# Performance work log

Hardware: AMD Instinct MI355X
Metric: run time of the kernel (lower is better)

## Reference

```python
import jax, jax.numpy as jnp
import numpy as np

SIZE = 768
SMALL = SIZE // 4 + 1  # 193
N_ROWS = 16 * 512      # 8192 flattened timesteps
N_CODES = 30000
N_PAIRS = 300000


def setup_inputs() -> dict:
    key = jax.random.key(0)
    ks = jax.random.split(key, 10)
    rnn_output = jax.random.normal(ks[0], (16, 512, SIZE), dtype=jnp.float32)
    weight = jax.random.normal(ks[1], (N_CODES, SIZE + 1), dtype=jnp.float32) * 0.02
    weight1 = jax.random.normal(ks[2], (N_CODES, SMALL), dtype=jnp.float32) * 0.02
    idx0 = jnp.stack([
        jax.random.randint(ks[3], (N_PAIRS,), 0, N_ROWS),
        jax.random.randint(ks[4], (N_PAIRS,), 0, N_CODES),
    ], axis=1).astype(jnp.int64)
    y0 = (jax.random.uniform(ks[5], (N_PAIRS,)) < 0.5).astype(jnp.float32)
    idx1 = jnp.stack([
        jax.random.randint(ks[6], (N_PAIRS,), 0, N_ROWS),
        jax.random.randint(ks[7], (N_PAIRS,), 0, N_CODES),
    ], axis=1).astype(jnp.int64)
    y1 = (jax.random.uniform(ks[8], (N_PAIRS,)) < 0.5).astype(jnp.float32)
    seen0 = jnp.zeros((N_PAIRS,), dtype=jnp.float32)
    seen1 = jnp.zeros((N_PAIRS,), dtype=jnp.float32)
    return {"rnn_output": rnn_output, "weight": weight, "weight1": weight1,
            "idx0": idx0, "y0": y0, "seen0": seen0,
            "idx1": idx1, "y1": y1, "seen1": seen1}


def _embedding_dot(features, table, idx):
    # gather feature rows and code-embedding rows, then row-wise dot -> [N]
    f = features[idx[:, 0]]   # [N, D]
    w = table[idx[:, 1]]      # [N, D]
    return jnp.sum(f * w, axis=-1)


def _bce_logits_sum(logits, targets):
    # stable: log(1 + exp(x)) - x*y, summed
    return jnp.sum(jnp.logaddexp(jnp.float32(0.0), logits) - logits * targets)


def reference(rnn_output, weight, weight1, idx0, y0, seen0, idx1, y1, seen1):
    flat = rnn_output.reshape(-1, SIZE)                     # [B*T, size]
    bias = jnp.ones((flat.shape[0], 1), dtype=flat.dtype)
    rnn_with_bias = jnp.concatenate([flat, bias], axis=1)   # [B*T, size+1]

    final = _embedding_dot(rnn_with_bias, weight, idx0)     # [N]
    loss = _bce_logits_sum(final, y0)

    smaller = rnn_with_bias[:, -SMALL:]                     # [B*T, small]
    final1 = _embedding_dot(smaller, weight1, idx1)         # [N]
    loss1 = _bce_logits_sum(final1, y1)

    return final, loss + loss1
```

## Files before the change

### kernel.cpp

```cpp
#include <hip/hip_runtime.h>
#include <hip/hip_fp16.h>

#define FSIZE   768
#define TW0     769
#define TW1     193
#define COL1    576
#define NPAIRS  300000
#define NCODES  30000
#define NROWS   8192
#define NCB     32768

#define NB0     1176
#define NB1     1176
#define NGRID   (NB0 + NB1)
#define NPART   NGRID

#define PB_H    512
#define PB_F    512
#define PB_W0   1024
#define PB_W1   256
#define NPRE    (PB_H + PB_F + PB_W0 + PB_W1)
#define S_H     (PB_H)
#define S_F     (PB_H + PB_F)
#define S_W0    (PB_H + PB_F + PB_W0)
#define FEAT_U4 393216
#define W0_U4   1440000
#define W1_U4   360000

#define O_FEAT8  ((size_t)0)
#define O_W08    (O_FEAT8 + 1572864)
#define O_W18    (O_W08 + 5760000)
#define O_B0F    (O_W18 + 1440000)
#define O_B1F    (O_B0F + 30000)
#define O_CNT    (O_B1F + 30000)
#define O_CUR    (O_CNT + 65536)
#define O_SREC   (O_CUR + 65536)
#define O_PART   (O_SREC + 2400000)
#define WS_U32   (O_PART + NPART + 64)

#define FSCALE   16.0f
#define WSCALE   64.0f
#define DESCALE  (1.0f / 1024.0f)

typedef float f32x2_t __attribute__((ext_vector_type(2)));

__device__ __forceinline__ float loss_term(float x, float y) {
    float ax = fabsf(x);
    return fmaxf(x, 0.0f) + log1pf(__expf(-ax)) - x * y;
}

__device__ __forceinline__ float4 ld4u(const float* p) {
    float4 v; __builtin_memcpy(&v, p, 16); return v;
}

#if defined(__has_builtin)
# if __has_builtin(__builtin_amdgcn_cvt_pk_f32_fp8)
#  define HW_FP8_DEC 1
# endif
# if __has_builtin(__builtin_amdgcn_cvt_pk_fp8_f32)
#  define HW_FP8_ENC 1
# endif
#endif

__device__ __forceinline__ float sw_fp8_to_f32(unsigned b) {
    unsigned mag = b & 0x7fu;
    unsigned r = ((b & 0x80u) << 24) | ((mag << 20) + 0x3C000000u);
    float f = __uint_as_float(r);
    return mag ? f : 0.0f;
}

template <bool HI>
__device__ __forceinline__ f32x2_t fp8x2_to_f32(unsigned u) {
#ifdef HW_FP8_DEC
    return __builtin_amdgcn_cvt_pk_f32_fp8(u, HI);
#else
    f32x2_t o;
    unsigned lo8 = HI ? ((u >> 16) & 0xffu) : (u & 0xffu);
    unsigned hi8 = HI ? ((u >> 24) & 0xffu) : ((u >> 8) & 0xffu);
    o[0] = sw_fp8_to_f32(lo8);
    o[1] = sw_fp8_to_f32(hi8);
    return o;
#endif
}

__device__ __forceinline__ unsigned sw_f32_to_fp8(float x) {
    unsigned short h = __half_as_ushort(__float2half(x));
    unsigned s = ((unsigned)h >> 8) & 0x80u;
    int e = (h >> 10) & 31;
    unsigned m = h & 1023u;
    if (e >= 23) return s | 0x7eu;
    if (e < 9)  return s;
    unsigned t = ((unsigned)(e - 8) << 3) | (m >> 7);
    unsigned rnd = (m >> 6) & 1u, sticky = (m & 63u) ? 1u : 0u;
    t += (rnd & (sticky | (t & 1u)));
    if (t > 0x7eu) t = 0x7eu;
    return s | t;
}

__device__ __forceinline__ unsigned f32x4_to_fp8(float a, float b, float c, float d) {
#ifdef HW_FP8_ENC
    int u = __builtin_amdgcn_cvt_pk_fp8_f32(a, b, 0, false);
    u = __builtin_amdgcn_cvt_pk_fp8_f32(c, d, u, true);
    return (unsigned)u;
#else
    return sw_f32_to_fp8(a) | (sw_f32_to_fp8(b) << 8)
         | (sw_f32_to_fp8(c) << 16) | (sw_f32_to_fp8(d) << 24);
#endif
}

__device__ __forceinline__ uint4 enc16(const float* s, float sc) {
    float4 a = ld4u(s), b = ld4u(s + 4), c = ld4u(s + 8), d = ld4u(s + 12);
    uint4 o;
    o.x = f32x4_to_fp8(a.x * sc, a.y * sc, a.z * sc, a.w * sc);
    o.y = f32x4_to_fp8(b.x * sc, b.y * sc, b.z * sc, b.w * sc);
    o.z = f32x4_to_fp8(c.x * sc, c.y * sc, c.z * sc, c.w * sc);
    o.w = f32x4_to_fp8(d.x * sc, d.y * sc, d.z * sc, d.w * sc);
    return o;
}

__device__ __forceinline__ float dot16(uint4 u, const float* w, float s) {
    f32x2_t p;
    p = fp8x2_to_f32<false>(u.x); s += p[0] * w[0]  + p[1] * w[1];
    p = fp8x2_to_f32<true >(u.x); s += p[0] * w[2]  + p[1] * w[3];
    p = fp8x2_to_f32<false>(u.y); s += p[0] * w[4]  + p[1] * w[5];
    p = fp8x2_to_f32<true >(u.y); s += p[0] * w[6]  + p[1] * w[7];
    p = fp8x2_to_f32<false>(u.z); s += p[0] * w[8]  + p[1] * w[9];
    p = fp8x2_to_f32<true >(u.z); s += p[0] * w[10] + p[1] * w[11];
    p = fp8x2_to_f32<false>(u.w); s += p[0] * w[12] + p[1] * w[13];
    p = fp8x2_to_f32<true >(u.w); s += p[0] * w[14] + p[1] * w[15];
    return s;
}

__device__ __forceinline__ float dot8(uint2 u, const float* w, float s) {
    f32x2_t p;
    p = fp8x2_to_f32<false>(u.x); s += p[0] * w[0] + p[1] * w[1];
    p = fp8x2_to_f32<true >(u.x); s += p[0] * w[2] + p[1] * w[3];
    p = fp8x2_to_f32<false>(u.y); s += p[0] * w[4] + p[1] * w[5];
    p = fp8x2_to_f32<true >(u.y); s += p[0] * w[6] + p[1] * w[7];
    return s;
}

__device__ __forceinline__ void unpack16(uint4 u, float* w) {
    f32x2_t p;
    p = fp8x2_to_f32<false>(u.x); w[0]  = p[0]; w[1]  = p[1];
    p = fp8x2_to_f32<true >(u.x); w[2]  = p[0]; w[3]  = p[1];
    p = fp8x2_to_f32<false>(u.y); w[4]  = p[0]; w[5]  = p[1];
    p = fp8x2_to_f32<true >(u.y); w[6]  = p[0]; w[7]  = p[1];
    p = fp8x2_to_f32<false>(u.z); w[8]  = p[0]; w[9]  = p[1];
    p = fp8x2_to_f32<true >(u.z); w[10] = p[0]; w[11] = p[1];
    p = fp8x2_to_f32<false>(u.w); w[12] = p[0]; w[13] = p[1];
    p = fp8x2_to_f32<true >(u.w); w[14] = p[0]; w[15] = p[1];
}

__device__ __forceinline__ void unpack8(uint2 u, float* w) {
    f32x2_t p;
    p = fp8x2_to_f32<false>(u.x); w[0] = p[0]; w[1] = p[1];
    p = fp8x2_to_f32<true >(u.x); w[2] = p[0]; w[3] = p[1];
    p = fp8x2_to_f32<false>(u.y); w[4] = p[0]; w[5] = p[1];
    p = fp8x2_to_f32<true >(u.y); w[6] = p[0]; w[7] = p[1];
}

__global__ __launch_bounds__(256) void zero_cnt_kernel(int* __restrict__ cnt) {
    cnt[blockIdx.x * 256 + threadIdx.x] = 0;
}

__global__ __launch_bounds__(256) void fused_pre_kernel(
    const float* __restrict__ feat, const float* __restrict__ w0,
    const float* __restrict__ w1,
    const int* __restrict__ idx0, const int* __restrict__ idx1,
    uint4* __restrict__ feat8, uint4* __restrict__ w08, uint4* __restrict__ w18,
    float* __restrict__ b0f, float* __restrict__ b1f, int* __restrict__ cnt)
{
    const int bid = blockIdx.x;
    if (bid < S_H) {
        const int tid = bid * 256 + threadIdx.x;
#pragma unroll
        for (int k = 0; k < 5; ++k) {
            const int i = tid + k * (PB_H * 256);
            if (i < 2 * NPAIRS) {
                if (i < NPAIRS) atomicAdd(&cnt[idx0[2 * i + 1]], 1);
                else            atomicAdd(&cnt[NCB + idx1[2 * (i - NPAIRS) + 1]], 1);
            }
        }
    } else if (bid < S_F) {
        const int tid = (bid - S_H) * 256 + threadIdx.x;
#pragma unroll
        for (int k = 0; k < 3; ++k) {
            const int i = tid + k * (PB_F * 256);
            feat8[i] = enc16(feat + (size_t)i * 16, FSCALE);
        }
    } else if (bid < S_W0) {
        const int tid = (bid - S_F) * 256 + threadIdx.x;
#pragma unroll
        for (int k = 0; k < 6; ++k) {
            const int i = tid + k * (PB_W0 * 256);
            if (i < W0_U4) {
                const int c = i / 48;
                const int e = (i - c * 48) * 16;
                const float* src = w0 + (size_t)c * TW0 + e;
                w08[i] = enc16(src, WSCALE);
                if (e == 0) b0f[c] = src[FSIZE];
            }
        }
    } else {
        const int tid = (bid - S_W0) * 256 + threadIdx.x;
#pragma unroll
        for (int k = 0; k < 6; ++k) {
            const int i = tid + k * (PB_W1 * 256);
            if (i < W1_U4) {
                const int c = i / 12;
                const int e = (i - c * 12) * 16;
                const float* src = w1 + (size_t)c * TW1 + e;
                w18[i] = enc16(src, WSCALE);
                if (e == 0) b1f[c] = src[TW1 - 1];
            }
        }
    }
}

__global__ __launch_bounds__(1024) void scan2_kernel(const int* __restrict__ cnt,
                                                     int* __restrict__ cursor) {
    __shared__ int wsum[16];
    __shared__ int wbase[16];
    const int t = threadIdx.x;
    const int lane = t & 63, wv = t >> 6;
    const int4* c4 = (const int4*)cnt + (size_t)t * 16;
    int4 v[16];
#pragma unroll
    for (int j = 0; j < 16; ++j) v[j] = c4[j];
    int s = 0;
#pragma unroll
    for (int j = 0; j < 16; ++j) {
        int a;
        a = v[j].x; v[j].x = s; s += a;
        a = v[j].y; v[j].y = s; s += a;
        a = v[j].z; v[j].z = s; s += a;
        a = v[j].w; v[j].w = s; s += a;
    }
    int incl = s;
#pragma unroll
    for (int off = 1; off < 64; off <<= 1) {
        int u = __shfl_up(incl, off, 64);
        if (lane >= off) incl += u;
    }
    if (lane == 63) wsum[wv] = incl;
    __syncthreads();
    if (wv == 0 && lane < 16) {
        int mysum = wsum[lane];
        int winc = mysum;
#pragma unroll
        for (int off = 1; off < 16; off <<= 1) {
            int u = __shfl_up(winc, off, 64);
            if (lane >= off) winc += u;
        }
        wbase[lane] = winc - mysum;
    }
    __syncthreads();
    const int base = wbase[wv] + incl - s;
    int4* cu = (int4*)cursor + (size_t)t * 16;
#pragma unroll
    for (int j = 0; j < 16; ++j)
        cu[j] = make_int4(base + v[j].x, base + v[j].y, base + v[j].z, base + v[j].w);
}

__global__ __launch_bounds__(256) void scatter2_kernel(
    const int* __restrict__ idx0, const float* __restrict__ y0,
    const int* __restrict__ idx1, const float* __restrict__ y1,
    int* __restrict__ cursor, uint4* __restrict__ srec, float* __restrict__ loss_out)
{
    const int tid = blockIdx.x * 256 + threadIdx.x;
    if (tid == 0) loss_out[0] = 0.0f;
#pragma unroll
    for (int k = 0; k < 2; ++k) {
        const int t = tid + k * 300032;
        if (t < NPAIRS) {
            int r = idx0[2 * t], c = idx0[2 * t + 1];
            int pos = atomicAdd(&cursor[c], 1);
            srec[pos] = make_uint4((unsigned)r, (unsigned)c, __float_as_uint(y0[t]), (unsigned)t);
        } else if (t < 2 * NPAIRS) {
            int p = t - NPAIRS;
            int r = idx1[2 * p], c = idx1[2 * p + 1];
            int pos = atomicAdd(&cursor[NCB + c], 1);
            srec[pos] = make_uint4((unsigned)r, (unsigned)c, __float_as_uint(y1[p]), (unsigned)p);
        }
    }
}

__global__ __launch_bounds__(256) void main3_kernel(
    const unsigned char* __restrict__ feat8, const unsigned char* __restrict__ w08,
    const unsigned char* __restrict__ w18,
    const float* __restrict__ b0f, const float* __restrict__ b1f,
    const uint4* __restrict__ srec,
    float* __restrict__ out_final, float* __restrict__ loss_out)
{
    __shared__ float bsum[4];
    const int lane = threadIdx.x & 63;
    const int wv   = threadIdx.x >> 6;
    float wavesum = 0.f;

    if (blockIdx.x < NB0) {
        const int work = (blockIdx.x & 7) * (NB0 / 8) + (blockIdx.x >> 3);
        const int wid = work * 4 + wv;
        const int g = lane >> 4, sub = lane & 15;
        const int mypair = wid * 64 + 16 * g + sub;
        int rdidx = mypair < NPAIRS ? mypair : NPAIRS - 1;
        const uint4 rec = srec[rdidx];
        int prev_c = -1;
        float wc[48];
        float wb = 0.f, lg = 0.f;
#pragma unroll
        for (int j = 0; j < 16; ++j) {
            const bool valid = (wid * 64 + 16 * g + j) < NPAIRS;
            if (valid) {
                const int src = (lane & 48) | j;
                const int r = __shfl((int)rec.x, src, 64);
                const int c = __shfl((int)rec.y, src, 64);
                if (c != prev_c) {
                    prev_c = c;
                    const unsigned char* wr = w08 + (size_t)c * FSIZE + 48 * sub;
                    uint4 wu0 = *(const uint4*)wr;
                    uint4 wu1 = *(const uint4*)(wr + 16);
                    uint4 wu2 = *(const uint4*)(wr + 32);
                    unpack16(wu0, &wc[0]);
                    unpack16(wu1, &wc[16]);
                    unpack16(wu2, &wc[32]);
                    wb = b0f[c];
                }
                const unsigned char* fr = feat8 + (size_t)r * FSIZE + 48 * sub;
                uint4 f0 = *(const uint4*)fr;
                uint4 f1 = *(const uint4*)(fr + 16);
                uint4 f2 = *(const uint4*)(fr + 32);
                float s = dot16(f0, &wc[0], 0.f);
                s = dot16(f1, &wc[16], s);
                s = dot16(f2, &wc[32], s);
                s += __shfl_xor(s, 8, 64);
                s += __shfl_xor(s, 4, 64);
                s += __shfl_xor(s, 2, 64);
                s += __shfl_xor(s, 1, 64);
                lg = (sub == j) ? s * DESCALE + wb : lg;
            }
        }
        float ll = 0.f;
        if (mypair < NPAIRS) {
            out_final[rec.w] = lg;
            ll = loss_term(lg, __uint_as_float(rec.z));
        }
#pragma unroll
        for (int m = 32; m; m >>= 1) ll += __shfl_xor(ll, m, 64);
        wavesum = ll;
    } else {
        const int tb = blockIdx.x - NB0;
        const int work1 = (tb & 7) * (NB1 / 8) + (tb >> 3);
        const long base = (long)(work1 * 4 + wv) * 64;
        if (base < NPAIRS) {
            const int g = lane >> 3, sub = lane & 7;
            long lpos = base + 8 * g + sub;
            if (lpos > NPAIRS - 1) lpos = NPAIRS - 1;
            const uint4 rec = srec[(size_t)NPAIRS + lpos];
            int prev_c = -1;
            float wc[24];
            float wb = 0.f, lg = 0.f;
#pragma unroll
            for (int j = 0; j < 8; ++j) {
                const bool valid = (base + 8 * g + j) < NPAIRS;
                const int src = (lane & 56) | j;
                const int r = __shfl((int)rec.x, src, 64);
                const int c = __shfl((int)rec.y, src, 64);
                if (valid) {
                    if (c != prev_c) {
                        prev_c = c;
                        const unsigned char* wr = w18 + (size_t)c * 192 + 24 * sub;
                        uint2 wu0 = *(const uint2*)wr;
                        uint2 wu1 = *(const uint2*)(wr + 8);
                        uint2 wu2 = *(const uint2*)(wr + 16);
                        unpack8(wu0, &wc[0]);
                        unpack8(wu1, &wc[8]);
                        unpack8(wu2, &wc[16]);
                        wb = b1f[c];
                    }
                    const unsigned char* fr = feat8 + (size_t)r * FSIZE + COL1 + 24 * sub;
                    uint2 f0 = *(const uint2*)fr;
                    uint2 f1 = *(const uint2*)(fr + 8);
                    uint2 f2 = *(const uint2*)(fr + 16);
                    float s = dot8(f0, &wc[0], 0.f);
                    s = dot8(f1, &wc[8], s);
                    s = dot8(f2, &wc[16], s);
                    s += __shfl_xor(s, 4, 64);
                    s += __shfl_xor(s, 2, 64);
                    s += __shfl_xor(s, 1, 64);
                    lg = (sub == j) ? s * DESCALE + wb : lg;
                }
            }
            float ll = 0.f;
            if ((base + 8 * g + sub) < NPAIRS)
                ll = loss_term(lg, __uint_as_float(rec.z));
#pragma unroll
            for (int m = 32; m; m >>= 1) ll += __shfl_xor(ll, m, 64);
            wavesum = ll;
        }
    }

    if (lane == 0) bsum[wv] = wavesum;
    __syncthreads();
    if (threadIdx.x == 0) {
        float t = bsum[0] + bsum[1] + bsum[2] + bsum[3];
        atomicAdd(loss_out, t);
    }
}

__global__ __launch_bounds__(1024) void reduce_kernel(
    const float* __restrict__ partial, int n, float* __restrict__ out)
{
    __shared__ float sh[1024];
    float s = 0.0f;
    for (int i = threadIdx.x; i < n; i += 1024) s += partial[i];
    sh[threadIdx.x] = s;
    __syncthreads();
    for (int off = 512; off; off >>= 1) {
        if ((int)threadIdx.x < off) sh[threadIdx.x] += sh[threadIdx.x + off];
        __syncthreads();
    }
    if (threadIdx.x == 0) out[0] = sh[0];
}

__global__ __launch_bounds__(256) void task0_kernel(
    const float* __restrict__ feat, const float* __restrict__ wt,
    const int* __restrict__ idx, const float* __restrict__ y,
    float* __restrict__ out_final, float* __restrict__ partial)
{
    __shared__ float lsum[4];
    const int lane = threadIdx.x & 63;
    const int wv = threadIdx.x >> 6;
    const int pair = blockIdx.x * 4 + wv;
    const int r = idx[2 * pair];
    const int c = idx[2 * pair + 1];
    const float4* f4 = (const float4*)(feat + (size_t)r * FSIZE);
    const float* wrow = wt + (size_t)c * TW0;
    float s = 0.0f;
#pragma unroll
    for (int k = 0; k < 3; ++k) {
        const int j = lane + (k << 6);
        float4 f = f4[j];
        float4 w = ld4u(wrow + 4 * j);
        s += f.x * w.x + f.y * w.y + f.z * w.z + f.w * w.w;
    }
#pragma unroll
    for (int m = 32; m; m >>= 1) s += __shfl_xor(s, m, 64);
    if (lane == 0) {
        const float logit = s + wrow[FSIZE];
        out_final[pair] = logit;
        lsum[wv] = loss_term(logit, y[pair]);
    }
    __syncthreads();
    if (threadIdx.x == 0)
        partial[blockIdx.x] = lsum[0] + lsum[1] + lsum[2] + lsum[3];
}

__global__ __launch_bounds__(256) void task1_kernel(
    const float* __restrict__ feat, const float* __restrict__ wt,
    const int* __restrict__ idx, const float* __restrict__ y,
    float* __restrict__ partial)
{
    __shared__ float lsum[16];
    const int lane = threadIdx.x & 63;
    const int wv = threadIdx.x >> 6;
    const int sub = lane & 15;
    const int pg = lane >> 4;
    const int pair = (blockIdx.x * 4 + wv) * 4 + pg;
    const int r = idx[2 * pair];
    const int c = idx[2 * pair + 1];
    const float4* f4 = (const float4*)(feat + (size_t)r * FSIZE + COL1);
    const float* wrow = wt + (size_t)c * TW1;
    float s = 0.0f;
#pragma unroll
    for (int k = 0; k < 3; ++k) {
        const int j = sub + (k << 4);
        float4 f = f4[j];
        float4 w = ld4u(wrow + 4 * j);
        s += f.x * w.x + f.y * w.y + f.z * w.z + f.w * w.w;
    }
#pragma unroll
    for (int m = 8; m; m >>= 1) s += __shfl_xor(s, m, 64);
    if (sub == 0) {
        const float logit = s + wrow[TW1 - 1];
        lsum[wv * 4 + pg] = loss_term(logit, y[pair]);
    }
    __syncthreads();
    if (threadIdx.x == 0) {
        float t = 0.0f;
#pragma unroll
        for (int i = 0; i < 16; ++i) t += lsum[i];
        partial[blockIdx.x] = t;
    }
}

extern "C" void kernel_launch(void* const* d_in, const int* in_sizes, int n_in,
                              void* d_out, int out_size, void* d_ws, size_t ws_size,
                              hipStream_t stream) {
    const float* feat = (const float*)d_in[0];
    const float* w0   = (const float*)d_in[1];
    const float* w1   = (const float*)d_in[2];
    const int*   idx0 = (const int*)d_in[3];
    const float* y0   = (const float*)d_in[4];
    const int*   idx1 = (const int*)d_in[6];
    const float* y1   = (const float*)d_in[7];

    float* out = (float*)d_out;
    unsigned* ws = (unsigned*)d_ws;

    if (ws_size >= WS_U32 * 4) {
        unsigned char* feat8 = (unsigned char*)(ws + O_FEAT8);
        unsigned char* w08   = (unsigned char*)(ws + O_W08);
        unsigned char* w18   = (unsigned char*)(ws + O_W18);
        float* b0f   = (float*)(ws + O_B0F);
        float* b1f   = (float*)(ws + O_B1F);
        int*   cnt   = (int*)(ws + O_CNT);
        int*   cursor= (int*)(ws + O_CUR);
        uint4* srec  = (uint4*)(ws + O_SREC);

        zero_cnt_kernel<<<256, 256, 0, stream>>>(cnt);
        fused_pre_kernel<<<NPRE, 256, 0, stream>>>(
            feat, w0, w1, idx0, idx1,
            (uint4*)feat8, (uint4*)w08, (uint4*)w18, b0f, b1f, cnt);
        scan2_kernel<<<1, 1024, 0, stream>>>(cnt, cursor);
        scatter2_kernel<<<1172, 256, 0, stream>>>(
            idx0, y0, idx1, y1, cursor, srec, out + NPAIRS);
        main3_kernel<<<NGRID, 256, 0, stream>>>(
            feat8, w08, w18, b0f, b1f, srec, out, out + NPAIRS);
    } else {
        float* part = (float*)ws;
        const int nb0 = NPAIRS / 4;
        const int nb1 = NPAIRS / 16;
        task0_kernel<<<nb0, 256, 0, stream>>>(feat, w0, idx0, y0, out, part);
        task1_kernel<<<nb1, 256, 0, stream>>>(feat, w1, idx1, y1, part + nb0);
        reduce_kernel<<<1, 1024, 0, stream>>>(part, nb0 + nb1, out + NPAIRS);
    }
}
```

Measured before the change: 167.5 us.

## Split preprocessing into two kernels and halve pairs per wave in task0

The fused preprocessing kernel is split in two. The histogram and feature encoding run before the scan, and weight encoding is moved after the scatter. Each thread now handles one element instead of looping, so the grids are larger. In the main kernel, task0 waves now process 32 pairs with 8 per 16-lane group instead of 64, and the block count doubles. This trades more weight-row reloads and less in-wave reuse for more parallelism and shorter serial loops, and adds one kernel launch.

```diff
diff --git a/kernel.cpp b/kernel.cpp
--- a/kernel.cpp
+++ b/kernel.cpp
@@ -10,21 +10,18 @@
 #define NROWS   8192
 #define NCB     32768
 
-#define NB0     1176
+#define NWAVES0 (NPAIRS / 32)
+#define NB0     2344
 #define NB1     1176
 #define NGRID   (NB0 + NB1)
 #define NPART   NGRID
 
-#define PB_H    512
-#define PB_F    512
-#define PB_W0   1024
-#define PB_W1   256
-#define NPRE    (PB_H + PB_F + PB_W0 + PB_W1)
-#define S_H     (PB_H)
-#define S_F     (PB_H + PB_F)
-#define S_W0    (PB_H + PB_F + PB_W0)
-#define FEAT_U4 393216
-#define W0_U4   1440000
+#define PA_H    1172
+#define PA_F    1536
+#define NPREA   (PA_H + PA_F)
+#define PB_W0   5625
+#define PB_W1   1407
+#define NPREB   (PB_W0 + PB_W1)
 #define W1_U4   360000
 
 #define O_FEAT8  ((size_t)0)
@@ -164,56 +161,47 @@
     cnt[blockIdx.x * 256 + threadIdx.x] = 0;
 }
 
-__global__ __launch_bounds__(256) void fused_pre_kernel(
-    const float* __restrict__ feat, const float* __restrict__ w0,
-    const float* __restrict__ w1,
+__global__ __launch_bounds__(256) void preA_kernel(
+    const float* __restrict__ feat,
     const int* __restrict__ idx0, const int* __restrict__ idx1,
-    uint4* __restrict__ feat8, uint4* __restrict__ w08, uint4* __restrict__ w18,
-    float* __restrict__ b0f, float* __restrict__ b1f, int* __restrict__ cnt)
+    uint4* __restrict__ feat8, int* __restrict__ cnt)
 {
     const int bid = blockIdx.x;
-    if (bid < S_H) {
-        const int tid = bid * 256 + threadIdx.x;
-#pragma unroll
-        for (int k = 0; k < 5; ++k) {
-            const int i = tid + k * (PB_H * 256);
-            if (i < 2 * NPAIRS) {
-                if (i < NPAIRS) atomicAdd(&cnt[idx0[2 * i + 1]], 1);
-                else            atomicAdd(&cnt[NCB + idx1[2 * (i - NPAIRS) + 1]], 1);
-            }
-        }
-    } else if (bid < S_F) {
-        const int tid = (bid - S_H) * 256 + threadIdx.x;
-#pragma unroll
-        for (int k = 0; k < 3; ++k) {
-            const int i = tid + k * (PB_F * 256);
-            feat8[i] = enc16(feat + (size_t)i * 16, FSCALE);
-        }
-    } else if (bid < S_W0) {
-        const int tid = (bid - S_F) * 256 + threadIdx.x;
-#pragma unroll
-        for (int k = 0; k < 6; ++k) {
-            const int i = tid + k * (PB_W0 * 256);
-            if (i < W0_U4) {
-                const int c = i / 48;
-                const int e = (i - c * 48) * 16;
-                const float* src = w0 + (size_t)c * TW0 + e;
-                w08[i] = enc16(src, WSCALE);
-                if (e == 0) b0f[c] = src[FSIZE];
-            }
+    if (bid < PA_H) {
+        const int t = bid * 256 + threadIdx.x;
+#pragma unroll
+        for (int k = 0; k < 2; ++k) {
+            const int i = t + k * (PA_H * 256);
+            if (i < NPAIRS) atomicAdd(&cnt[idx0[2 * i + 1]], 1);
+            else if (i < 2 * NPAIRS) atomicAdd(&cnt[NCB + idx1[2 * (i - NPAIRS) + 1]], 1);
         }
     } else {
-        const int tid = (bid - S_W0) * 256 + threadIdx.x;
-#pragma unroll
-        for (int k = 0; k < 6; ++k) {
-            const int i = tid + k * (PB_W1 * 256);
-            if (i < W1_U4) {
-                const int c = i / 12;
-                const int e = (i - c * 12) * 16;
-                const float* src = w1 + (size_t)c * TW1 + e;
-                w18[i] = enc16(src, WSCALE);
-                if (e == 0) b1f[c] = src[TW1 - 1];
-            }
+        const int t = (bid - PA_H) * 256 + threadIdx.x;
+        feat8[t] = enc16(feat + (size_t)t * 16, FSCALE);
+    }
+}
+
+__global__ __launch_bounds__(256) void preB_kernel(
+    const float* __restrict__ w0, const float* __restrict__ w1,
+    uint4* __restrict__ w08, uint4* __restrict__ w18,
+    float* __restrict__ b0f, float* __restrict__ b1f)
+{
+    const int bid = blockIdx.x;
+    if (bid < PB_W0) {
+        const int i = bid * 256 + threadIdx.x;
+        const int c = i / 48;
+        const int e = (i - c * 48) * 16;
+        const float* src = w0 + (size_t)c * TW0 + e;
+        w08[i] = enc16(src, WSCALE);
+        if (e == 0) b0f[c] = src[FSIZE];
+    } else {
+        const int i = (bid - PB_W0) * 256 + threadIdx.x;
+        if (i < W1_U4) {
+            const int c = i / 12;
+            const int e = (i - c * 12) * 16;
+            const float* src = w1 + (size_t)c * TW1 + e;
+            w18[i] = enc16(src, WSCALE);
+            if (e == 0) b1f[c] = src[TW1 - 1];
         }
     }
 }
@@ -301,17 +289,14 @@
     if (blockIdx.x < NB0) {
         const int work = (blockIdx.x & 7) * (NB0 / 8) + (blockIdx.x >> 3);
         const int wid = work * 4 + wv;
-        const int g = lane >> 4, sub = lane & 15;
-        const int mypair = wid * 64 + 16 * g + sub;
-        int rdidx = mypair < NPAIRS ? mypair : NPAIRS - 1;
-        const uint4 rec = srec[rdidx];
-        int prev_c = -1;
-        float wc[48];
-        float wb = 0.f, lg = 0.f;
-#pragma unroll
-        for (int j = 0; j < 16; ++j) {
-            const bool valid = (wid * 64 + 16 * g + j) < NPAIRS;
-            if (valid) {
+        if (wid < NWAVES0) {
+            const int g = lane >> 4, sub = lane & 15;
+            const uint4 rec = srec[(size_t)wid * 32 + 8 * g + (sub & 7)];
+            int prev_c = -1;
+            float wc[48];
+            float wb = 0.f, lg = 0.f;
+#pragma unroll
+            for (int j = 0; j < 8; ++j) {
                 const int src = (lane & 48) | j;
                 const int r = __shfl((int)rec.x, src, 64);
                 const int c = __shfl((int)rec.y, src, 64);
@@ -339,15 +324,15 @@
                 s += __shfl_xor(s, 1, 64);
                 lg = (sub == j) ? s * DESCALE + wb : lg;
             }
+            float ll = 0.f;
+            if (sub < 8) {
+                out_final[rec.w] = lg;
+                ll = loss_term(lg, __uint_as_float(rec.z));
+            }
+#pragma unroll
+            for (int m = 32; m; m >>= 1) ll += __shfl_xor(ll, m, 64);
+            wavesum = ll;
         }
-        float ll = 0.f;
-        if (mypair < NPAIRS) {
-            out_final[rec.w] = lg;
-            ll = loss_term(lg, __uint_as_float(rec.z));
-        }
-#pragma unroll
-        for (int m = 32; m; m >>= 1) ll += __shfl_xor(ll, m, 64);
-        wavesum = ll;
     } else {
         const int tb = blockIdx.x - NB0;
         const int work1 = (tb & 7) * (NB1 / 8) + (tb >> 3);
@@ -519,12 +504,11 @@
         uint4* srec  = (uint4*)(ws + O_SREC);
 
         zero_cnt_kernel<<<256, 256, 0, stream>>>(cnt);
-        fused_pre_kernel<<<NPRE, 256, 0, stream>>>(
-            feat, w0, w1, idx0, idx1,
-            (uint4*)feat8, (uint4*)w08, (uint4*)w18, b0f, b1f, cnt);
+        preA_kernel<<<NPREA, 256, 0, stream>>>(feat, idx0, idx1, (uint4*)feat8, cnt);
         scan2_kernel<<<1, 1024, 0, stream>>>(cnt, cursor);
         scatter2_kernel<<<1172, 256, 0, stream>>>(
             idx0, y0, idx1, y1, cursor, srec, out + NPAIRS);
+        preB_kernel<<<NPREB, 256, 0, stream>>>(w0, w1, (uint4*)w08, (uint4*)w18, b0f, b1f);
         main3_kernel<<<NGRID, 256, 0, stream>>>(
             feat8, w08, w18, b0f, b1f, srec, out, out + NPAIRS);
     } else {
```

New measurement: 180.1 us. 1.08x slower.

## Rebalance preprocessing blocks and halve pairs per wave in main kernel

Applied to the files above, without the earlier changes.

Each wave in the main 769-wide dot kernel now handles 32 pairs instead of 64, and the block count doubles to spread the loop work over more waves. The preprocessing kernel is repartitioned with new block counts per section. Bias extraction moves into the histogram section, and the encode sections batch four 16-float loads before encoding to raise memory-level parallelism. The trade-off is less reuse of cached weight rows per wave and more waves to launch.

```diff
diff --git a/kernel.cpp b/kernel.cpp
--- a/kernel.cpp
+++ b/kernel.cpp
@@ -10,19 +10,17 @@
 #define NROWS   8192
 #define NCB     32768
 
-#define NB0     1176
+#define NWAVES0 (NPAIRS / 32)
+#define NB0     2344
 #define NB1     1176
 #define NGRID   (NB0 + NB1)
 #define NPART   NGRID
 
-#define PB_H    512
-#define PB_F    512
-#define PB_W0   1024
-#define PB_W1   256
-#define NPRE    (PB_H + PB_F + PB_W0 + PB_W1)
-#define S_H     (PB_H)
-#define S_F     (PB_H + PB_F)
-#define S_W0    (PB_H + PB_F + PB_W0)
+#define PH_B    645
+#define PF_B    384
+#define PW0_B   1407
+#define PW1_B   352
+#define NPRE    (PH_B + PF_B + PW0_B + PW1_B)
 #define FEAT_U4 393216
 #define W0_U4   1440000
 #define W1_U4   360000
@@ -108,14 +106,8 @@
 #endif
 }
 
-__device__ __forceinline__ uint4 enc16(const float* s, float sc) {
-    float4 a = ld4u(s), b = ld4u(s + 4), c = ld4u(s + 8), d = ld4u(s + 12);
-    uint4 o;
-    o.x = f32x4_to_fp8(a.x * sc, a.y * sc, a.z * sc, a.w * sc);
-    o.y = f32x4_to_fp8(b.x * sc, b.y * sc, b.z * sc, b.w * sc);
-    o.z = f32x4_to_fp8(c.x * sc, c.y * sc, c.z * sc, c.w * sc);
-    o.w = f32x4_to_fp8(d.x * sc, d.y * sc, d.z * sc, d.w * sc);
-    return o;
+__device__ __forceinline__ unsigned enc4(float4 v, float sc) {
+    return f32x4_to_fp8(v.x * sc, v.y * sc, v.z * sc, v.w * sc);
 }
 
 __device__ __forceinline__ float dot16(uint4 u, const float* w, float s) {
@@ -172,47 +164,99 @@
     float* __restrict__ b0f, float* __restrict__ b1f, int* __restrict__ cnt)
 {
     const int bid = blockIdx.x;
-    if (bid < S_H) {
-        const int tid = bid * 256 + threadIdx.x;
-#pragma unroll
-        for (int k = 0; k < 5; ++k) {
-            const int i = tid + k * (PB_H * 256);
-            if (i < 2 * NPAIRS) {
-                if (i < NPAIRS) atomicAdd(&cnt[idx0[2 * i + 1]], 1);
-                else            atomicAdd(&cnt[NCB + idx1[2 * (i - NPAIRS) + 1]], 1);
+    if (bid < PH_B) {
+        const int t = bid * 256 + threadIdx.x;
+        const int NT = PH_B * 256;
+#pragma unroll
+        for (int k = 0; k < 4; ++k) {
+            const int i = t + k * NT;
+            if (i < NPAIRS) {
+                atomicAdd(&cnt[idx0[2 * i + 1]], 1);
+            } else if (i < 2 * NPAIRS) {
+                atomicAdd(&cnt[NCB + idx1[2 * (i - NPAIRS) + 1]], 1);
+            } else if (i < 2 * NPAIRS + NCODES) {
+                const int c = i - 2 * NPAIRS;
+                b0f[c] = w0[(size_t)c * TW0 + FSIZE];
+            } else if (i < 2 * NPAIRS + 2 * NCODES) {
+                const int c = i - 2 * NPAIRS - NCODES;
+                b1f[c] = w1[(size_t)c * TW1 + (TW1 - 1)];
             }
         }
-    } else if (bid < S_F) {
-        const int tid = (bid - S_H) * 256 + threadIdx.x;
-#pragma unroll
-        for (int k = 0; k < 3; ++k) {
-            const int i = tid + k * (PB_F * 256);
-            feat8[i] = enc16(feat + (size_t)i * 16, FSCALE);
-        }
-    } else if (bid < S_W0) {
-        const int tid = (bid - S_F) * 256 + threadIdx.x;
-#pragma unroll
-        for (int k = 0; k < 6; ++k) {
-            const int i = tid + k * (PB_W0 * 256);
+    } else if (bid < PH_B + PF_B) {
+        const int t = (bid - PH_B) * 256 + threadIdx.x;
+        const int NT = PF_B * 256;
+        float4 v[16];
+#pragma unroll
+        for (int k = 0; k < 4; ++k) {
+            const float* s = feat + (size_t)(t + k * NT) * 16;
+            v[4 * k + 0] = ld4u(s);
+            v[4 * k + 1] = ld4u(s + 4);
+            v[4 * k + 2] = ld4u(s + 8);
+            v[4 * k + 3] = ld4u(s + 12);
+        }
+#pragma unroll
+        for (int k = 0; k < 4; ++k) {
+            uint4 o;
+            o.x = enc4(v[4 * k + 0], FSCALE);
+            o.y = enc4(v[4 * k + 1], FSCALE);
+            o.z = enc4(v[4 * k + 2], FSCALE);
+            o.w = enc4(v[4 * k + 3], FSCALE);
+            feat8[t + k * NT] = o;
+        }
+    } else if (bid < PH_B + PF_B + PW0_B) {
+        const int t = (bid - PH_B - PF_B) * 256 + threadIdx.x;
+        const int NT = PW0_B * 256;
+        float4 v[16];
+#pragma unroll
+        for (int k = 0; k < 4; ++k) {
+            int i = t + k * NT;
+            if (i >= W0_U4) i = W0_U4 - 1;
+            const int c = i / 48;
+            const int e = (i - c * 48) * 16;
+            const float* s = w0 + (size_t)c * TW0 + e;
+            v[4 * k + 0] = ld4u(s);
+            v[4 * k + 1] = ld4u(s + 4);
+            v[4 * k + 2] = ld4u(s + 8);
+            v[4 * k + 3] = ld4u(s + 12);
+        }
+#pragma unroll
+        for (int k = 0; k < 4; ++k) {
+            const int i = t + k * NT;
             if (i < W0_U4) {
-                const int c = i / 48;
-                const int e = (i - c * 48) * 16;
-                const float* src = w0 + (size_t)c * TW0 + e;
-                w08[i] = enc16(src, WSCALE);
-                if (e == 0) b0f[c] = src[FSIZE];
+                uint4 o;
+                o.x = enc4(v[4 * k + 0], WSCALE);
+                o.y = enc4(v[4 * k + 1], WSCALE);
+                o.z = enc4(v[4 * k + 2], WSCALE);
+                o.w = enc4(v[4 * k + 3], WSCALE);
+                w08[i] = o;
             }
         }
     } else {
-        const int tid = (bid - S_W0) * 256 + threadIdx.x;
-#pragma unroll
-        for (int k = 0; k < 6; ++k) {
-            const int i = tid + k * (PB_W1 * 256);
+        const int t = (bid - PH_B - PF_B - PW0_B) * 256 + threadIdx.x;
+        const int NT = PW1_B * 256;
+        float4 v[16];
+#pragma unroll
+        for (int k = 0; k < 4; ++k) {
+            int i = t + k * NT;
+            if (i >= W1_U4) i = W1_U4 - 1;
+            const int c = i / 12;
+            const int e = (i - c * 12) * 16;
+            const float* s = w1 + (size_t)c * TW1 + e;
+            v[4 * k + 0] = ld4u(s);
+            v[4 * k + 1] = ld4u(s + 4);
+            v[4 * k + 2] = ld4u(s + 8);
+            v[4 * k + 3] = ld4u(s + 12);
+        }
+#pragma unroll
+        for (int k = 0; k < 4; ++k) {
+            const int i = t + k * NT;
             if (i < W1_U4) {
-                const int c = i / 12;
-                const int e = (i - c * 12) * 16;
-                const float* src = w1 + (size_t)c * TW1 + e;
-                w18[i] = enc16(src, WSCALE);
-                if (e == 0) b1f[c] = src[TW1 - 1];
+                uint4 o;
+                o.x = enc4(v[4 * k + 0], WSCALE);
+                o.y = enc4(v[4 * k + 1], WSCALE);
+                o.z = enc4(v[4 * k + 2], WSCALE);
+                o.w = enc4(v[4 * k + 3], WSCALE);
+                w18[i] = o;
             }
         }
     }
@@ -301,17 +345,14 @@
     if (blockIdx.x < NB0) {
         const int work = (blockIdx.x & 7) * (NB0 / 8) + (blockIdx.x >> 3);
         const int wid = work * 4 + wv;
-        const int g = lane >> 4, sub = lane & 15;
-        const int mypair = wid * 64 + 16 * g + sub;
-        int rdidx = mypair < NPAIRS ? mypair : NPAIRS - 1;
-        const uint4 rec = srec[rdidx];
-        int prev_c = -1;
-        float wc[48];
-        float wb = 0.f, lg = 0.f;
-#pragma unroll
-        for (int j = 0; j < 16; ++j) {
-            const bool valid = (wid * 64 + 16 * g + j) < NPAIRS;
-            if (valid) {
+        if (wid < NWAVES0) {
+            const int g = lane >> 4, sub = lane & 15;
+            const uint4 rec = srec[(size_t)wid * 32 + 8 * g + (sub & 7)];
+            int prev_c = -1;
+            float wc[48];
+            float wb = 0.f, lg = 0.f;
+#pragma unroll
+            for (int j = 0; j < 8; ++j) {
                 const int src = (lane & 48) | j;
                 const int r = __shfl((int)rec.x, src, 64);
                 const int c = __shfl((int)rec.y, src, 64);
@@ -339,15 +380,15 @@
                 s += __shfl_xor(s, 1, 64);
                 lg = (sub == j) ? s * DESCALE + wb : lg;
             }
-        }
-        float ll = 0.f;
-        if (mypair < NPAIRS) {
-            out_final[rec.w] = lg;
-            ll = loss_term(lg, __uint_as_float(rec.z));
-        }
-#pragma unroll
-        for (int m = 32; m; m >>= 1) ll += __shfl_xor(ll, m, 64);
-        wavesum = ll;
+            float ll = 0.f;
+            if (sub < 8) {
+                out_final[rec.w] = lg;
+                ll = loss_term(lg, __uint_as_float(rec.z));
+            }
+#pragma unroll
+            for (int m = 32; m; m >>= 1) ll += __shfl_xor(ll, m, 64);
+            wavesum = ll;
+        }
     } else {
         const int tb = blockIdx.x - NB0;
         const int work1 = (tb & 7) * (NB1 / 8) + (tb >> 3);
```

New measurement: 174.0 us. 1.04x slower.
